# Kernel tuning notes

Hardware: AMD Instinct MI355X
Metric: run time of the kernel (lower is better)

Reference implementation:

```python
import jax, jax.numpy as jnp
import numpy as np

B, S, HID = 1, 2048, 4096
NH, NKV, D = 32, 8, 128          # query heads, kv heads, head_dim
GROUPS = NH // NKV               # GQA repeat factor = 4
WINDOW = 1024                    # sliding-window size
ROPE_BASE = 10000.0


def setup_inputs() -> dict:
    key = jax.random.key(0)
    k = jax.random.split(key, 5)
    hidden_states = jax.random.normal(k[0], (B, S, HID), jnp.float32)
    Wq = jax.random.normal(k[1], (HID, HID), jnp.float32) * 0.02
    Wk = jax.random.normal(k[2], (NKV * D, HID), jnp.float32) * 0.02
    Wv = jax.random.normal(k[3], (NKV * D, HID), jnp.float32) * 0.02
    Wo = jax.random.normal(k[4], (HID, HID), jnp.float32) * 0.02
    position_ids = jnp.arange(S, dtype=jnp.int64 if jax.config.jax_enable_x64 else jnp.int32)[None, :]
    # Sliding-window causal additive mask [B,1,S,S]: key j visible to query i iff i-WINDOW < j <= i
    i = jnp.arange(S)
    visible = (i[None, :] <= i[:, None]) & (i[:, None] - i[None, :] < WINDOW)
    neg = jnp.finfo(jnp.float32).min
    attention_mask = jnp.where(visible, 0.0, neg)[None, None, :, :].astype(jnp.float32)
    return {"hidden_states": hidden_states, "attention_mask": attention_mask,
            "position_ids": position_ids, "Wq": Wq, "Wk": Wk, "Wv": Wv, "Wo": Wo}


def _rotate_half(x):
    x1, x2 = x[..., : D // 2], x[..., D // 2:]
    return jnp.concatenate((-x2, x1), axis=-1)


def _rope_cos_sin(position_ids, dtype):
    # inv_freq over even dims; gather-by-position_ids == direct indexing
    inv_freq = 1.0 / (ROPE_BASE ** (jnp.arange(0, D, 2, dtype=jnp.float32) / D))  # [D/2]
    freqs = position_ids.astype(jnp.float32)[..., None] * inv_freq                # [B,S,D/2]
    emb = jnp.concatenate((freqs, freqs), axis=-1)                                # [B,S,D]
    cos = jnp.cos(emb)[:, None, :, :].astype(dtype)                               # [B,1,S,D]
    sin = jnp.sin(emb)[:, None, :, :].astype(dtype)
    return cos, sin


def reference(hidden_states, attention_mask, position_ids, Wq, Wk, Wv, Wo):
    bsz, q_len, _ = hidden_states.shape
    # projections (nn.Linear: y = x @ W.T)
    q = (hidden_states @ Wq.T).reshape(bsz, q_len, NH, D).transpose(0, 2, 1, 3)    # [B,NH,S,D]
    k = (hidden_states @ Wk.T).reshape(bsz, q_len, NKV, D).transpose(0, 2, 1, 3)   # [B,NKV,S,D]
    v = (hidden_states @ Wv.T).reshape(bsz, q_len, NKV, D).transpose(0, 2, 1, 3)
    cos, sin = _rope_cos_sin(position_ids, q.dtype)
    q = q * cos + _rotate_half(q) * sin
    k = k * cos + _rotate_half(k) * sin
    # GQA repeat_kv (repeat_interleave along head dim)
    k = jnp.repeat(k, GROUPS, axis=1)                                              # [B,NH,S,D]
    v = jnp.repeat(v, GROUPS, axis=1)
    scores = jnp.einsum('bhqd,bhkd->bhqk', q, k) / np.sqrt(D)                       # [B,NH,S,S]
    scores = scores + attention_mask
    scores = jnp.maximum(scores, jnp.finfo(scores.dtype).min)
    probs = jax.nn.softmax(scores.astype(jnp.float32), axis=-1).astype(q.dtype)
    out = jnp.einsum('bhqk,bhkd->bhqd', probs, v)                                   # [B,NH,S,D]
    out = out.transpose(0, 2, 1, 3).reshape(bsz, q_len, HID)
    return out @ Wo.T
```

## Files before the change

### kernel.cpp

```cpp
#include <hip/hip_runtime.h>

#define S_LEN 2048
#define HID   4096
#define NH    32
#define NKV   8
#define DH    128
#define KVD   (NKV*DH)
#define WIN   1024
#define NTOT  6144

typedef __bf16 bf16_t;
typedef __bf16 bfrag  __attribute__((ext_vector_type(8)));
typedef __bf16 bf4    __attribute__((ext_vector_type(4)));
typedef float  ffrag  __attribute__((ext_vector_type(4)));
typedef float  f4     __attribute__((ext_vector_type(4)));

__global__ __launch_bounds__(256) void f32_to_bf16_kernel(const float* __restrict__ src,
                                                          bf16_t* __restrict__ dst, int n4) {
  int i = blockIdx.x * 256 + threadIdx.x;
  if (i < n4) {
    ffrag v = *(const ffrag*)(src + (size_t)i * 4);
    bf4 o;
    o[0] = (bf16_t)v[0]; o[1] = (bf16_t)v[1]; o[2] = (bf16_t)v[2]; o[3] = (bf16_t)v[3];
    *(bf4*)(dst + (size_t)i * 4) = o;
  }
}

__global__ __launch_bounds__(256) void cvt4_kernel(const float* __restrict__ h,
    const float* __restrict__ Wq, const float* __restrict__ Wk, const float* __restrict__ Wv,
    bf16_t* __restrict__ hB, bf16_t* __restrict__ WqB,
    bf16_t* __restrict__ WkB, bf16_t* __restrict__ WvB) {
  int i = blockIdx.x * 256 + threadIdx.x;
  const int N0 = S_LEN * HID / 4;
  const int N1 = N0 + HID * HID / 4;
  const int N2 = N1 + KVD * HID / 4;
  const float* s; bf16_t* d; int off;
  if (i < N0)      { s = h;  d = hB;  off = i; }
  else if (i < N1) { s = Wq; d = WqB; off = i - N0; }
  else if (i < N2) { s = Wk; d = WkB; off = i - N1; }
  else             { s = Wv; d = WvB; off = i - N2; }
  ffrag v = *(const ffrag*)(s + (size_t)off * 4);
  bf4 o;
  o[0] = (bf16_t)v[0]; o[1] = (bf16_t)v[1]; o[2] = (bf16_t)v[2]; o[3] = (bf16_t)v[3];
  *(bf4*)(d + (size_t)off * 4) = o;
}


__device__ __forceinline__ void load_lds16(const bf16_t* g, bf16_t* l) {
  __builtin_amdgcn_global_load_lds((__attribute__((address_space(1))) void*)g,
                                   (__attribute__((address_space(3))) void*)l,
                                   16, 0, 0);
}

#define BARW() asm volatile("s_barrier" ::: "memory")
#define WAITV(n) asm volatile("s_waitcnt vmcnt(" #n ")" ::: "memory")
#define LGKM0() do { asm volatile("s_waitcnt lgkmcnt(0)" ::: "memory"); \
                     __builtin_amdgcn_sched_barrier(0); } while (0)

template <int BNR, int OUT_MODE>
__device__ __forceinline__ void gemm_body(const bf16_t* __restrict__ A,
                                          const bf16_t* __restrict__ B,
                                          void* __restrict__ Cv,
                                          int N, bf16_t* lds) {
  constexpr int K     = 4096;
  constexpr int NT    = K / 64;
  constexpr int NTF   = BNR / 64;
  constexpr int WC    = BNR / 4;
  constexpr int ABUFE = 128 * 64;
  constexpr int BBUFE = BNR * 64;

  bf16_t* As0 = lds;
  bf16_t* Bs0 = lds + 2 * ABUFE;

  const int raw  = blockIdx.x;
  const int xcd  = raw & 7;
  const int slot = raw >> 3;
  const int bx   = xcd * 4 + (slot & 3);
  const int by   = slot >> 2;
  const int row0 = by * 128;
  const int col0 = bx * BNR;

  const int tid  = threadIdx.x;
  const int wave = tid >> 6;
  const int lane = tid & 63;
  const int wr = wave >> 2, wc = wave & 3;
  const int n = lane & 15, qd = lane >> 4;

  const int rsub = tid >> 3;
  const int sg   = (tid & 7) ^ (rsub & 7);
  const bf16_t* Ag = A + (size_t)(row0 + rsub) * K + sg * 8;
  const bf16_t* Bg = B + (size_t)(col0 + rsub) * K + sg * 8;
  const int wbase = wave * 512;

  const int pg0 = ( qd      ^ (n & 7)) * 8;
  const int pg1 = ((4 | qd) ^ (n & 7)) * 8;
  const int abase = (wr * 64 + n) * 64;
  const int bbase = (wc * WC + n) * 64;

  ffrag acc[4][NTF];
#pragma unroll
  for (int mt = 0; mt < 4; ++mt)
#pragma unroll
    for (int nt = 0; nt < NTF; ++nt) {
      acc[mt][nt][0] = 0.f; acc[mt][nt][1] = 0.f; acc[mt][nt][2] = 0.f; acc[mt][nt][3] = 0.f;
    }

  auto STAGE = [&](int t, int s) {
    const int ko = t * 64;
    bf16_t* as = As0 + s * ABUFE + wbase;
    bf16_t* bs = Bs0 + s * BBUFE + wbase;
    load_lds16(Ag + ko, as);
    load_lds16(Ag + (size_t)64 * K + ko, as + 4096);
    load_lds16(Bg + ko, bs);
    load_lds16(Bg + (size_t)64 * K + ko, bs + 4096);
    if constexpr (BNR == 192) load_lds16(Bg + (size_t)128 * K + ko, bs + 8192);
  };

  STAGE(0, 0); STAGE(1, 1);
  if constexpr (BNR == 192) { WAITV(5); } else { WAITV(4); }
  BARW();

  for (int t = 0; t < NT; ++t) {
    const int s = t & 1;
    const bf16_t* Asl = As0 + s * ABUFE;
    const bf16_t* Bsl = Bs0 + s * BBUFE;
    bfrag av[4], bv[NTF];

#pragma unroll
    for (int mt = 0; mt < 4; ++mt) av[mt] = *(const bfrag*)(Asl + abase + mt * 1024 + pg0);
#pragma unroll
    for (int nt = 0; nt < NTF; ++nt) bv[nt] = *(const bfrag*)(Bsl + bbase + nt * 1024 + pg0);
    __builtin_amdgcn_s_setprio(1);
#pragma unroll
    for (int mt = 0; mt < 4; ++mt)
#pragma unroll
      for (int nt = 0; nt < NTF; ++nt)
        acc[mt][nt] = __builtin_amdgcn_mfma_f32_16x16x32_bf16(av[mt], bv[nt], acc[mt][nt], 0, 0, 0);
    __builtin_amdgcn_s_setprio(0);

#pragma unroll
    for (int mt = 0; mt < 4; ++mt) av[mt] = *(const bfrag*)(Asl + abase + mt * 1024 + pg1);
#pragma unroll
    for (int nt = 0; nt < NTF; ++nt) bv[nt] = *(const bfrag*)(Bsl + bbase + nt * 1024 + pg1);
    __builtin_amdgcn_s_setprio(1);
#pragma unroll
    for (int mt = 0; mt < 4; ++mt)
#pragma unroll
      for (int nt = 0; nt < NTF; ++nt)
        acc[mt][nt] = __builtin_amdgcn_mfma_f32_16x16x32_bf16(av[mt], bv[nt], acc[mt][nt], 0, 0, 0);
    __builtin_amdgcn_s_setprio(0);

    LGKM0();
    BARW();
    if (t + 2 < NT) STAGE(t + 2, s);
    if (t + 1 < NT) {
      if (t + 2 < NT) { if constexpr (BNR == 192) { WAITV(5); } else { WAITV(4); } }
      else            { WAITV(0); }
      BARW();
    }
  }

  const int orow = row0 + wr * 64 + qd * 4;
  const int ocol = col0 + wc * WC + n;
#pragma unroll
  for (int mt = 0; mt < 4; ++mt)
#pragma unroll
    for (int nt = 0; nt < NTF; ++nt)
#pragma unroll
      for (int r = 0; r < 4; ++r) {
        size_t idx = (size_t)(orow + mt * 16 + r) * N + (ocol + nt * 16);
        if (OUT_MODE == 1) ((bf16_t*)Cv)[idx] = (bf16_t)acc[mt][nt][r];
        else               ((float*)Cv)[idx]  = acc[mt][nt][r];
      }
}

__global__ __launch_bounds__(512, 4) void gemm_qkv_kernel(const bf16_t* __restrict__ hB,
                                                          const bf16_t* __restrict__ Wqkv,
                                                          bf16_t* __restrict__ C) {
  __shared__ __align__(16) bf16_t lds[2 * 128 * 64 + 2 * 192 * 64];
  gemm_body<192, 1>(hB, Wqkv, C, NTOT, lds);
}

__global__ __launch_bounds__(512, 4) void gemm_out_kernel(const bf16_t* __restrict__ A,
                                                          const bf16_t* __restrict__ B,
                                                          float* __restrict__ out) {
  __shared__ __align__(16) bf16_t lds[2 * 128 * 64 + 2 * 128 * 64];
  gemm_body<128, 0>(A, B, out, HID, lds);
}

__global__ __launch_bounds__(256) void ropecvt_kernel(const bf16_t* __restrict__ Cqkv,
                                                      bf16_t* __restrict__ Qb,
                                                      bf16_t* __restrict__ Kb,
                                                      bf16_t* __restrict__ Vb) {
  int idx = blockIdx.x * 256 + threadIdx.x;
  int g  = idx & 7;
  int t  = idx >> 3;
  int hh = t % 48;
  int s  = t / 48;
  const bf16_t* r0 = Cqkv + (size_t)s * NTOT + hh * 128;
  bfrag a0 = *(const bfrag*)&r0[g * 8];
  bfrag a1 = *(const bfrag*)&r0[g * 8 + 64];
  bf16_t* p;
  bool rope;
  if (hh < NH)           { p = Qb + (size_t)s * HID + hh * DH;        rope = true; }
  else if (hh < NH+NKV)  { p = Kb + (size_t)s * KVD + (hh - NH) * DH; rope = true; }
  else                   { p = Vb + (size_t)s * KVD + (hh - 40) * DH; rope = false; }
  bfrag o1, o2;
#pragma unroll
  for (int j = 0; j < 8; ++j) {
    float x1 = (float)a0[j];
    float x2 = (float)a1[j];
    if (rope) {
      int d = g * 8 + j;
      float inv = exp2f((float)d * (-13.287712379549449f / 64.f));
      float ang = (float)s * inv;
      float sn = sinf(ang), cs = cosf(ang);
      o1[j] = (bf16_t)(x1 * cs - x2 * sn);
      o2[j] = (bf16_t)(x2 * cs + x1 * sn);
    } else {
      o1[j] = (bf16_t)x1;
      o2[j] = (bf16_t)x2;
    }
  }
  *(bfrag*)&p[g * 8]      = o1;
  *(bfrag*)&p[g * 8 + 64] = o2;
}

#define KS_STRIDE 136
#define VT_STRIDE 72
#define PS_STRIDE 72

__global__ __launch_bounds__(256, 3) void attn_kernel(const bf16_t* __restrict__ Q,
                                                      const bf16_t* __restrict__ Kc,
                                                      const bf16_t* __restrict__ Vc,
                                                      bf16_t* __restrict__ AO) {
  const int qt   = 31 - blockIdx.x;
  const int h    = blockIdx.y;
  const int kvh  = h >> 2;
  const int q0   = qt * 64;
  const int tid  = threadIdx.x;
  const int wq   = tid >> 6;
  const int lane = tid & 63;
  const int n    = lane & 15;
  const int quad = lane >> 4;
  const float scale = 0.08838834764831845f;

  __shared__ __align__(16) bf16_t Ks[64 * KS_STRIDE];
  __shared__ __align__(16) bf16_t VT[128 * VT_STRIDE];
  __shared__ __align__(16) bf16_t Ps[4][16 * PS_STRIDE];

  bfrag aq[4];
#pragma unroll
  for (int kc = 0; kc < 4; ++kc) {
    bfrag t = *(const bfrag*)&Q[(size_t)(q0 + wq * 16 + n) * HID + h * DH + kc * 32 + quad * 8];
#pragma unroll
    for (int e = 0; e < 8; ++e) t[e] = (bf16_t)((float)t[e] * scale);
    aq[kc] = t;
  }

  ffrag acc[8];
#pragma unroll
  for (int dt = 0; dt < 8; ++dt) { acc[dt][0] = 0.f; acc[dt][1] = 0.f; acc[dt][2] = 0.f; acc[dt][3] = 0.f; }
  float lrow[4] = {0.f, 0.f, 0.f, 0.f};

  const int ktlo = (q0 >= WIN) ? ((q0 - (WIN - 1)) >> 6) : 0;
  const int kthi = (q0 + 63) >> 6;

  const int kg = tid & 15;
  const int dg = tid >> 4;

  bfrag pk[4], pv[4];
  {
    const int k0 = ktlo * 64;
#pragma unroll
    for (int i = 0; i < 4; ++i) {
      int pos = i * 256 + tid;
      pk[i] = *(const bfrag*)&Kc[(size_t)(k0 + (pos >> 4)) * KVD + kvh * DH + (pos & 15) * 8];
    }
#pragma unroll
    for (int j = 0; j < 4; ++j)
      pv[j] = *(const bfrag*)&Vc[(size_t)(k0 + j * 16 + kg) * KVD + kvh * DH + dg * 8];
  }

  for (int kt = ktlo; kt <= kthi; ++kt) {
    const int k0 = kt * 64;
    __syncthreads();
#pragma unroll
    for (int i = 0; i < 4; ++i) {
      int pos = i * 256 + tid;
      *(bfrag*)&Ks[(pos >> 4) * KS_STRIDE + (pos & 15) * 8] = pk[i];
    }
#pragma unroll
    for (int i = 0; i < 8; ++i) {
      bf4 pkk;
      pkk[0] = pv[0][i]; pkk[1] = pv[1][i]; pkk[2] = pv[2][i]; pkk[3] = pv[3][i];
      *(bf4*)&VT[(dg * 8 + i) * VT_STRIDE + kg * 4] = pkk;
    }
    __syncthreads();
    if (kt < kthi) {
      const int k1 = k0 + 64;
#pragma unroll
      for (int i = 0; i < 4; ++i) {
        int pos = i * 256 + tid;
        pk[i] = *(const bfrag*)&Kc[(size_t)(k1 + (pos >> 4)) * KVD + kvh * DH + (pos & 15) * 8];
      }
#pragma unroll
      for (int j = 0; j < 4; ++j)
        pv[j] = *(const bfrag*)&Vc[(size_t)(k1 + j * 16 + kg) * KVD + kvh * DH + dg * 8];
    }

    ffrag s[4];
#pragma unroll
    for (int nt = 0; nt < 4; ++nt) { s[nt][0] = 0.f; s[nt][1] = 0.f; s[nt][2] = 0.f; s[nt][3] = 0.f; }
#pragma unroll
    for (int kc = 0; kc < 4; ++kc) {
      bfrag bk[4];
#pragma unroll
      for (int nt = 0; nt < 4; ++nt)
        bk[nt] = *(const bfrag*)&Ks[(nt * 16 + n) * KS_STRIDE + kc * 32 + quad * 8];
#pragma unroll
      for (int nt = 0; nt < 4; ++nt)
        s[nt] = __builtin_amdgcn_mfma_f32_16x16x32_bf16(aq[kc], bk[nt], s[nt], 0, 0, 0);
    }

    const bool full = (k0 + 63 <= q0) && (q0 + 63 - k0 < WIN);
    if (!full) {
#pragma unroll
      for (int nt = 0; nt < 4; ++nt)
#pragma unroll
        for (int r = 0; r < 4; ++r) {
          int q = q0 + wq * 16 + quad * 4 + r;
          int k = k0 + nt * 16 + n;
          bool vis = (k <= q) && ((q - k) < WIN);
          if (!vis) s[nt][r] = -1e30f;
        }
    }

#pragma unroll
    for (int r = 0; r < 4; ++r) {
      bf4 pkk;
      float ps0 = __expf(s[0][r]);
      float ps1 = __expf(s[1][r]);
      float ps2 = __expf(s[2][r]);
      float ps3 = __expf(s[3][r]);
      lrow[r] += (ps0 + ps1) + (ps2 + ps3);
      pkk[0] = (bf16_t)ps0; pkk[1] = (bf16_t)ps1; pkk[2] = (bf16_t)ps2; pkk[3] = (bf16_t)ps3;
      *(bf4*)&Ps[wq][(quad * 4 + r) * PS_STRIDE + n * 4] = pkk;
    }

#pragma unroll
    for (int kc = 0; kc < 2; ++kc) {
      bfrag ap = *(const bfrag*)&Ps[wq][n * PS_STRIDE + kc * 32 + quad * 8];
#pragma unroll
      for (int dt = 0; dt < 8; ++dt) {
        bfrag bv = *(const bfrag*)&VT[(dt * 16 + n) * VT_STRIDE + kc * 32 + quad * 8];
        acc[dt] = __builtin_amdgcn_mfma_f32_16x16x32_bf16(ap, bv, acc[dt], 0, 0, 0);
      }
    }
  }

#pragma unroll
  for (int off = 1; off < 16; off <<= 1)
#pragma unroll
    for (int r = 0; r < 4; ++r) lrow[r] += __shfl_xor(lrow[r], off);
  float inv[4];
#pragma unroll
  for (int r = 0; r < 4; ++r) inv[r] = 1.f / lrow[r];
#pragma unroll
  for (int dt = 0; dt < 8; ++dt)
#pragma unroll
    for (int r = 0; r < 4; ++r)
      AO[(size_t)(q0 + wq * 16 + quad * 4 + r) * HID + h * DH + dt * 16 + n] =
          (bf16_t)(acc[dt][r] * inv[r]);
}

extern "C" void kernel_launch(void* const* d_in, const int* in_sizes, int n_in,
                              void* d_out, int out_size, void* d_ws, size_t ws_size,
                              hipStream_t stream) {
  const float* h  = (const float*)d_in[0];
  const float* Wq = (const float*)d_in[3];
  const float* Wk = (const float*)d_in[4];
  const float* Wv = (const float*)d_in[5];
  const float* Wo = (const float*)d_in[6];
  float* out = (float*)d_out;

  char* ws = (char*)d_ws;
  const size_t MB = (size_t)1 << 20;
  bf16_t* hB    = (bf16_t*)(ws + 0 * MB);
  bf16_t* Qb    = (bf16_t*)(ws + 0 * MB);
  bf16_t* WqB   = (bf16_t*)(ws + 16 * MB);
  bf16_t* WkB   = (bf16_t*)(ws + 48 * MB);
  bf16_t* WvB   = (bf16_t*)(ws + 56 * MB);
  bf16_t* Cqkv  = (bf16_t*)(ws + 64 * MB);
  bf16_t* WoB   = (bf16_t*)(ws + 64 * MB);
  bf16_t* AOb   = (bf16_t*)(ws + 96 * MB);
  bf16_t* Kb    = (bf16_t*)(ws + 112 * MB);
  bf16_t* Vb    = (bf16_t*)(ws + 116 * MB);

  cvt4_kernel<<<(S_LEN * HID + HID * HID + 2 * KVD * HID) / 4 / 256, 256, 0, stream>>>(
      h, Wq, Wk, Wv, hB, WqB, WkB, WvB);

  gemm_qkv_kernel<<<512, 512, 0, stream>>>(hB, WqB, Cqkv);

  ropecvt_kernel<<<(S_LEN * 48 * 8) / 256, 256, 0, stream>>>(Cqkv, Qb, Kb, Vb);

  f32_to_bf16_kernel<<<(HID * HID / 4 + 255) / 256, 256, 0, stream>>>(Wo, WoB, HID * HID / 4);

  attn_kernel<<<dim3(32, NH), 256, 0, stream>>>(Qb, Kb, Vb, AOb);

  gemm_out_kernel<<<512, 512, 0, stream>>>(AOb, WoB, out);
}
```

Measured before the change: 454.4 us.

## Enlarge GEMM tiles to 256 rows and split-K the output projection with atomics

Both GEMMs now use 256-row M tiles with eight 16-row MFMA fragments per wave, which doubles register accumulators and halves the grid. The output projection uses 256x256 tiles and splits K into two halves, with results combined through float atomicAdd after a memset of the output. The aim is more reuse of each loaded tile and a better-filled grid for the output GEMM. In exchange it lowers occupancy (launch bounds 2), adds atomic traffic and a memset, and makes the float summation order nondeterministic.

```diff
diff --git a/kernel.cpp b/kernel.cpp
--- a/kernel.cpp
+++ b/kernel.cpp
@@ -57,135 +57,140 @@
 #define LGKM0() do { asm volatile("s_waitcnt lgkmcnt(0)" ::: "memory"); \
                      __builtin_amdgcn_sched_barrier(0); } while (0)
 
-template <int BNR, int OUT_MODE>
+template <int BN, int NT, int OUT_MODE>
 __device__ __forceinline__ void gemm_body(const bf16_t* __restrict__ A,
                                           const bf16_t* __restrict__ B,
                                           void* __restrict__ Cv,
+                                          int row0, int col0, int kbeg,
                                           int N, bf16_t* lds) {
   constexpr int K     = 4096;
-  constexpr int NT    = K / 64;
-  constexpr int NTF   = BNR / 64;
-  constexpr int WC    = BNR / 4;
-  constexpr int ABUFE = 128 * 64;
-  constexpr int BBUFE = BNR * 64;
+  constexpr int WC    = BN / 4;
+  constexpr int NTF   = WC / 16;
+  constexpr int BSW   = BN / 64;
+  constexpr int ABUFE = 256 * 64;
+  constexpr int BBUFE = BN * 64;
 
   bf16_t* As0 = lds;
   bf16_t* Bs0 = lds + 2 * ABUFE;
 
+  const int tid  = threadIdx.x;
+  const int wave = tid >> 6;
+  const int lane = tid & 63;
+  const int wr = wave >> 2, wc = wave & 3;
+  const int n = lane & 15, qd = lane >> 4;
+
+  const int rsub = tid >> 3;
+  const int sg   = (tid & 7) ^ (rsub & 7);
+  const bf16_t* Ag = A + (size_t)(row0 + rsub) * K + sg * 8;
+  const bf16_t* Bg = B + (size_t)(col0 + rsub) * K + sg * 8;
+  const int wbase = wave * 512;
+
+  const int pg0 = ( qd      ^ (n & 7)) * 8;
+  const int pg1 = ((4 | qd) ^ (n & 7)) * 8;
+  const int abase = (wr * 128 + n) * 64;
+  const int bbase = (wc * WC + n) * 64;
+
+  ffrag acc[8][NTF];
+#pragma unroll
+  for (int mt = 0; mt < 8; ++mt)
+#pragma unroll
+    for (int nt = 0; nt < NTF; ++nt) {
+      acc[mt][nt][0] = 0.f; acc[mt][nt][1] = 0.f; acc[mt][nt][2] = 0.f; acc[mt][nt][3] = 0.f;
+    }
+
+  auto STAGE = [&](int t, int s) {
+    const int ko = kbeg + t * 64;
+    bf16_t* as = As0 + s * ABUFE + wbase;
+    bf16_t* bs = Bs0 + s * BBUFE + wbase;
+#pragma unroll
+    for (int i = 0; i < 4; ++i)
+      load_lds16(Ag + (size_t)(i * 64) * K + ko, as + i * 4096);
+#pragma unroll
+    for (int i = 0; i < BSW; ++i)
+      load_lds16(Bg + (size_t)(i * 64) * K + ko, bs + i * 4096);
+  };
+
+  STAGE(0, 0); STAGE(1, 1);
+  if constexpr (BN == 192) { WAITV(7); } else { WAITV(8); }
+  BARW();
+
+  for (int t = 0; t < NT; ++t) {
+    const int s = t & 1;
+    const bf16_t* Asl = As0 + s * ABUFE;
+    const bf16_t* Bsl = Bs0 + s * BBUFE;
+    bfrag av[8], bv[NTF];
+
+#pragma unroll
+    for (int mt = 0; mt < 8; ++mt) av[mt] = *(const bfrag*)(Asl + abase + mt * 1024 + pg0);
+#pragma unroll
+    for (int nt = 0; nt < NTF; ++nt) bv[nt] = *(const bfrag*)(Bsl + bbase + nt * 1024 + pg0);
+    __builtin_amdgcn_s_setprio(1);
+#pragma unroll
+    for (int mt = 0; mt < 8; ++mt)
+#pragma unroll
+      for (int nt = 0; nt < NTF; ++nt)
+        acc[mt][nt] = __builtin_amdgcn_mfma_f32_16x16x32_bf16(av[mt], bv[nt], acc[mt][nt], 0, 0, 0);
+    __builtin_amdgcn_s_setprio(0);
+
+#pragma unroll
+    for (int mt = 0; mt < 8; ++mt) av[mt] = *(const bfrag*)(Asl + abase + mt * 1024 + pg1);
+#pragma unroll
+    for (int nt = 0; nt < NTF; ++nt) bv[nt] = *(const bfrag*)(Bsl + bbase + nt * 1024 + pg1);
+    __builtin_amdgcn_s_setprio(1);
+#pragma unroll
+    for (int mt = 0; mt < 8; ++mt)
+#pragma unroll
+      for (int nt = 0; nt < NTF; ++nt)
+        acc[mt][nt] = __builtin_amdgcn_mfma_f32_16x16x32_bf16(av[mt], bv[nt], acc[mt][nt], 0, 0, 0);
+    __builtin_amdgcn_s_setprio(0);
+
+    LGKM0();
+    BARW();
+    if (t + 2 < NT) STAGE(t + 2, s);
+    if (t + 1 < NT) {
+      if (t + 2 < NT) { if constexpr (BN == 192) { WAITV(7); } else { WAITV(8); } }
+      else            { WAITV(0); }
+      BARW();
+    }
+  }
+
+  const int orow = row0 + wr * 128 + qd * 4;
+  const int ocol = col0 + wc * WC + n;
+#pragma unroll
+  for (int mt = 0; mt < 8; ++mt)
+#pragma unroll
+    for (int nt = 0; nt < NTF; ++nt)
+#pragma unroll
+      for (int r = 0; r < 4; ++r) {
+        size_t idx = (size_t)(orow + mt * 16 + r) * N + (ocol + nt * 16);
+        if (OUT_MODE == 1) ((bf16_t*)Cv)[idx] = (bf16_t)acc[mt][nt][r];
+        else               atomicAdd(&((float*)Cv)[idx], acc[mt][nt][r]);
+      }
+}
+
+__global__ __launch_bounds__(512, 2) void gemm_qkv_kernel(const bf16_t* __restrict__ hB,
+                                                          const bf16_t* __restrict__ Wqkv,
+                                                          bf16_t* __restrict__ C) {
+  __shared__ __align__(16) bf16_t lds[2 * 256 * 64 + 2 * 192 * 64];
   const int raw  = blockIdx.x;
   const int xcd  = raw & 7;
   const int slot = raw >> 3;
   const int bx   = xcd * 4 + (slot & 3);
   const int by   = slot >> 2;
-  const int row0 = by * 128;
-  const int col0 = bx * BNR;
-
-  const int tid  = threadIdx.x;
-  const int wave = tid >> 6;
-  const int lane = tid & 63;
-  const int wr = wave >> 2, wc = wave & 3;
-  const int n = lane & 15, qd = lane >> 4;
-
-  const int rsub = tid >> 3;
-  const int sg   = (tid & 7) ^ (rsub & 7);
-  const bf16_t* Ag = A + (size_t)(row0 + rsub) * K + sg * 8;
-  const bf16_t* Bg = B + (size_t)(col0 + rsub) * K + sg * 8;
-  const int wbase = wave * 512;
-
-  const int pg0 = ( qd      ^ (n & 7)) * 8;
-  const int pg1 = ((4 | qd) ^ (n & 7)) * 8;
-  const int abase = (wr * 64 + n) * 64;
-  const int bbase = (wc * WC + n) * 64;
-
-  ffrag acc[4][NTF];
-#pragma unroll
-  for (int mt = 0; mt < 4; ++mt)
-#pragma unroll
-    for (int nt = 0; nt < NTF; ++nt) {
-      acc[mt][nt][0] = 0.f; acc[mt][nt][1] = 0.f; acc[mt][nt][2] = 0.f; acc[mt][nt][3] = 0.f;
-    }
-
-  auto STAGE = [&](int t, int s) {
-    const int ko = t * 64;
-    bf16_t* as = As0 + s * ABUFE + wbase;
-    bf16_t* bs = Bs0 + s * BBUFE + wbase;
-    load_lds16(Ag + ko, as);
-    load_lds16(Ag + (size_t)64 * K + ko, as + 4096);
-    load_lds16(Bg + ko, bs);
-    load_lds16(Bg + (size_t)64 * K + ko, bs + 4096);
-    if constexpr (BNR == 192) load_lds16(Bg + (size_t)128 * K + ko, bs + 8192);
-  };
-
-  STAGE(0, 0); STAGE(1, 1);
-  if constexpr (BNR == 192) { WAITV(5); } else { WAITV(4); }
-  BARW();
-
-  for (int t = 0; t < NT; ++t) {
-    const int s = t & 1;
-    const bf16_t* Asl = As0 + s * ABUFE;
-    const bf16_t* Bsl = Bs0 + s * BBUFE;
-    bfrag av[4], bv[NTF];
-
-#pragma unroll
-    for (int mt = 0; mt < 4; ++mt) av[mt] = *(const bfrag*)(Asl + abase + mt * 1024 + pg0);
-#pragma unroll
-    for (int nt = 0; nt < NTF; ++nt) bv[nt] = *(const bfrag*)(Bsl + bbase + nt * 1024 + pg0);
-    __builtin_amdgcn_s_setprio(1);
-#pragma unroll
-    for (int mt = 0; mt < 4; ++mt)
-#pragma unroll
-      for (int nt = 0; nt < NTF; ++nt)
-        acc[mt][nt] = __builtin_amdgcn_mfma_f32_16x16x32_bf16(av[mt], bv[nt], acc[mt][nt], 0, 0, 0);
-    __builtin_amdgcn_s_setprio(0);
-
-#pragma unroll
-    for (int mt = 0; mt < 4; ++mt) av[mt] = *(const bfrag*)(Asl + abase + mt * 1024 + pg1);
-#pragma unroll
-    for (int nt = 0; nt < NTF; ++nt) bv[nt] = *(const bfrag*)(Bsl + bbase + nt * 1024 + pg1);
-    __builtin_amdgcn_s_setprio(1);
-#pragma unroll
-    for (int mt = 0; mt < 4; ++mt)
-#pragma unroll
-      for (int nt = 0; nt < NTF; ++nt)
-        acc[mt][nt] = __builtin_amdgcn_mfma_f32_16x16x32_bf16(av[mt], bv[nt], acc[mt][nt], 0, 0, 0);
-    __builtin_amdgcn_s_setprio(0);
-
-    LGKM0();
-    BARW();
-    if (t + 2 < NT) STAGE(t + 2, s);
-    if (t + 1 < NT) {
-      if (t + 2 < NT) { if constexpr (BNR == 192) { WAITV(5); } else { WAITV(4); } }
-      else            { WAITV(0); }
-      BARW();
-    }
-  }
-
-  const int orow = row0 + wr * 64 + qd * 4;
-  const int ocol = col0 + wc * WC + n;
-#pragma unroll
-  for (int mt = 0; mt < 4; ++mt)
-#pragma unroll
-    for (int nt = 0; nt < NTF; ++nt)
-#pragma unroll
-      for (int r = 0; r < 4; ++r) {
-        size_t idx = (size_t)(orow + mt * 16 + r) * N + (ocol + nt * 16);
-        if (OUT_MODE == 1) ((bf16_t*)Cv)[idx] = (bf16_t)acc[mt][nt][r];
-        else               ((float*)Cv)[idx]  = acc[mt][nt][r];
-      }
-}
-
-__global__ __launch_bounds__(512, 4) void gemm_qkv_kernel(const bf16_t* __restrict__ hB,
-                                                          const bf16_t* __restrict__ Wqkv,
-                                                          bf16_t* __restrict__ C) {
-  __shared__ __align__(16) bf16_t lds[2 * 128 * 64 + 2 * 192 * 64];
-  gemm_body<192, 1>(hB, Wqkv, C, NTOT, lds);
-}
-
-__global__ __launch_bounds__(512, 4) void gemm_out_kernel(const bf16_t* __restrict__ A,
+  gemm_body<192, 64, 1>(hB, Wqkv, C, by * 256, bx * 192, 0, NTOT, lds);
+}
+
+__global__ __launch_bounds__(512, 2) void gemm_out_kernel(const bf16_t* __restrict__ A,
                                                           const bf16_t* __restrict__ B,
                                                           float* __restrict__ out) {
-  __shared__ __align__(16) bf16_t lds[2 * 128 * 64 + 2 * 128 * 64];
-  gemm_body<128, 0>(A, B, out, HID, lds);
+  __shared__ __align__(16) bf16_t lds[2 * 256 * 64 + 2 * 256 * 64];
+  const int raw  = blockIdx.x;
+  const int xcd  = raw & 7;
+  const int slot = raw >> 3;
+  const int bx   = xcd * 2 + (slot & 1);
+  const int by   = (slot >> 1) & 7;
+  const int kz   = slot >> 4;
+  gemm_body<256, 32, 2>(A, B, out, by * 256, bx * 256, kz * 2048, HID, lds);
 }
 
 __global__ __launch_bounds__(256) void ropecvt_kernel(const bf16_t* __restrict__ Cqkv,
@@ -400,7 +405,7 @@
   cvt4_kernel<<<(S_LEN * HID + HID * HID + 2 * KVD * HID) / 4 / 256, 256, 0, stream>>>(
       h, Wq, Wk, Wv, hB, WqB, WkB, WvB);
 
-  gemm_qkv_kernel<<<512, 512, 0, stream>>>(hB, WqB, Cqkv);
+  gemm_qkv_kernel<<<256, 512, 0, stream>>>(hB, WqB, Cqkv);
 
   ropecvt_kernel<<<(S_LEN * 48 * 8) / 256, 256, 0, stream>>>(Cqkv, Qb, Kb, Vb);
 
@@ -408,5 +413,7 @@
 
   attn_kernel<<<dim3(32, NH), 256, 0, stream>>>(Qb, Kb, Vb, AOb);
 
-  gemm_out_kernel<<<512, 512, 0, stream>>>(AOb, WoB, out);
-}
+  hipMemsetAsync(out, 0, (size_t)S_LEN * HID * sizeof(float), stream);
+
+  gemm_out_kernel<<<256, 512, 0, stream>>>(AOb, WoB, out);
+}
```

New measurement: 493.8 us. 1.09x slower.
